# Optimization experiments

Measured on AMD Instinct MI355X. Metric: run time of the kernel, lower is better.

Reference implementation:

```python
import jax, jax.numpy as jnp
import numpy as np

N_CLASSES = 2048
NUM_GROUP = 8
CLS_PER_GROUP = N_CLASSES // NUM_GROUP  # 256
NUM_SAMPLE = 10
EMB_DIM = 400
COMMITMENT = 0.25


def setup_inputs() -> dict:
    key = jax.random.key(0)
    k1, k2 = jax.random.split(key)
    x0 = jax.random.normal(k1, (64, 512, 1, EMB_DIM), dtype=jnp.float32)
    emb = jax.random.normal(k2, (N_CLASSES, EMB_DIM), dtype=jnp.float32)
    return {"x0": x0, "emb": emb}


def reference(x0, emb):
    x = x0  # normalize=False path
    M = x0.shape[0] * x0.shape[1] * x0.shape[2]
    x1 = x.reshape(M, EMB_DIM)

    # pairwise squared distances [M, N_CLASSES]
    d = (jnp.sum(x1 ** 2, axis=1, keepdims=True)
         + jnp.sum(emb ** 2, axis=1)
         - 2.0 * x1 @ emb.T)

    # per-group mean distance -> group argmin
    d_g = d.reshape(M, NUM_GROUP, CLS_PER_GROUP)
    group = jnp.argmin(jnp.mean(d_g, axis=2), axis=1)  # [M]

    # inverse-distance probs restricted to the chosen group
    d_sel = jnp.take_along_axis(d_g, group[:, None, None], axis=1)[:, 0, :]  # [M, CLS_PER_GROUP]
    prob_sel = 1.0 / d_sel
    p, idx_local = jax.lax.top_k(prob_sel, NUM_SAMPLE)  # descending, [M, NUM_SAMPLE]
    index = group[:, None] * CLS_PER_GROUP + idx_local  # global codebook indices

    # L1 normalize kept probabilities (F.normalize p=1)
    prob_dist = p / jnp.maximum(jnp.sum(jnp.abs(p), axis=1, keepdims=True), 1e-12)

    # entropy of top-1 code histogram
    hist = jnp.bincount(index[:, 0], length=N_CLASSES).astype(jnp.float32)
    pr = hist / jnp.float32(M)
    entropy = -jnp.sum(jnp.where(hist > 0, pr * jnp.log(jnp.where(hist > 0, pr, 1.0)), 0.0))

    # weighted gather-sum of code vectors (probs are detached in original)
    gathered = emb[index]  # [M, NUM_SAMPLE, EMB_DIM]
    w = jax.lax.stop_gradient(prob_dist)[:, :, None]
    output = jnp.sum(gathered * w, axis=1).reshape(x.shape)

    out0 = jax.lax.stop_gradient(output - x) + x  # straight-through
    q_latent = jnp.mean((jax.lax.stop_gradient(x) - output) ** 2)
    e_latent = jnp.mean((x - jax.lax.stop_gradient(output)) ** 2)
    loss = q_latent + COMMITMENT * e_latent

    encodings = (1.0 / d)[None]  # [1, M, N_CLASSES]
    return (loss, out0, entropy, encodings)
```

## Files before the change

kernel.cpp:

```cpp
#include <hip/hip_runtime.h>
#include <math.h>

#define M_ROWS 32768
#define N_CLS  2048
#define NGRP   8
#define CPG    256
#define NS     10
#define NCAND  16
#define EDIM   400
#define KPAD   416
#define NKT    13
#define BK     32
#define SGS    448
#define NPART  32

typedef _Float16 f16x8 __attribute__((ext_vector_type(8)));
typedef float f32x4 __attribute__((ext_vector_type(4)));

__device__ __forceinline__ void gld_lds16(const void* g, void* l) {
    __builtin_amdgcn_global_load_lds(
        (const __attribute__((address_space(1))) unsigned int*)g,
        (__attribute__((address_space(3))) unsigned int*)l, 16, 0, 0);
}

__global__ __launch_bounds__(256) void k_split_hi(const float* __restrict__ in,
                                                  unsigned short* __restrict__ hi,
                                                  float* __restrict__ ss, int rows) {
    int row  = blockIdx.x * 4 + (threadIdx.x >> 6);
    int lane = threadIdx.x & 63;
    if (row >= rows) return;
    const float* src = in + (size_t)row * EDIM;
    unsigned short* ph = hi + (size_t)row * KPAD;
    float s = 0.f;
    #pragma unroll
    for (int q = 0; q < 2; ++q) {
        int c4 = lane + q * 64;
        if (c4 < KPAD / 4) {
            int k = c4 * 4;
            float4 v = make_float4(0.f, 0.f, 0.f, 0.f);
            if (k < EDIM) v = *(const float4*)(src + k);
            float va[4] = {v.x, v.y, v.z, v.w};
            unsigned short ha[4];
            #pragma unroll
            for (int t = 0; t < 4; ++t) {
                float f = va[t];
                _Float16 h = (_Float16)f;
                ha[t] = __builtin_bit_cast(unsigned short, h);
                s = fmaf(f, f, s);
            }
            ushort4 H; H.x = ha[0]; H.y = ha[1]; H.z = ha[2]; H.w = ha[3];
            *(ushort4*)(ph + k) = H;
        }
    }
    #pragma unroll
    for (int o = 32; o; o >>= 1) s += __shfl_xor(s, o, 64);
    if (lane == 0) ss[row] = s;
}

__global__ __launch_bounds__(448) void k_groupsum(const float* __restrict__ emb,
                                                  const unsigned short* __restrict__ ehi,
                                                  float* __restrict__ Sg,
                                                  float* __restrict__ SgH) {
    const int g = blockIdx.x;
    const int t = threadIdx.x;
    float se = 0.f, sh = 0.f;
    if (t < EDIM) {
        for (int j = 0; j < CPG; ++j) {
            se += emb[(size_t)(g * CPG + j) * EDIM + t];
            _Float16 h = __builtin_bit_cast(_Float16, ehi[(size_t)(g * CPG + j) * KPAD + t]);
            sh += (float)h;
        }
    }
    Sg[g * SGS + t]  = se;
    SgH[g * SGS + t] = sh;
}

__global__ __launch_bounds__(256, 4) void k_dist1(
    const unsigned short* __restrict__ xhi, const unsigned short* __restrict__ ehi,
    const float* __restrict__ xx, const float* __restrict__ ee,
    float* __restrict__ enc, float* __restrict__ gsum) {
    __shared__ __attribute__((aligned(16))) _Float16 Ah[128][BK];
    __shared__ __attribute__((aligned(16))) _Float16 Bh[128][BK];

    const int wg    = blockIdx.x;
    const int xcd   = wg & 7;
    const int local = wg >> 3;
    const int mx    = xcd * 32 + (local & 31);
    const int ny    = local >> 5;
    const int m0    = mx * 128;
    const int n0    = ny * 128;

    const int tid  = threadIdx.x;
    const int lane = tid & 63, wid = tid >> 6;
    const int wr = (wid >> 1) * 64, wc = (wid & 1) * 64;
    const int lr = lane & 15, ko = lane >> 4;

    f32x4 acc[4][4];
    #pragma unroll
    for (int i = 0; i < 4; ++i)
        #pragma unroll
        for (int j = 0; j < 4; ++j) { f32x4 z = {0.f, 0.f, 0.f, 0.f}; acc[i][j] = z; }

    for (int kt = 0; kt < NKT; ++kt) {
        const int k0 = kt * BK;
        #pragma unroll
        for (int q = 0; q < 2; ++q) {
            int c = q * 256 + tid;
            int row = c >> 2, kc = c & 3;
            size_t goA = (size_t)(m0 + row) * KPAD + k0 + kc * 8;
            size_t goB = (size_t)(n0 + row) * KPAD + k0 + kc * 8;
            int loff = (c >> 6) * 1024;
            gld_lds16(xhi + goA, (char*)&Ah[0][0] + loff);
            gld_lds16(ehi + goB, (char*)&Bh[0][0] + loff);
        }
        __syncthreads();

        f16x8 a_h[4];
        #pragma unroll
        for (int i = 0; i < 4; ++i)
            a_h[i] = *(const f16x8*)&Ah[wr + i * 16 + lr][ko * 8];
        #pragma unroll
        for (int j = 0; j < 4; ++j) {
            f16x8 b_h = *(const f16x8*)&Bh[wc + j * 16 + lr][ko * 8];
            #pragma unroll
            for (int i = 0; i < 4; ++i)
                acc[i][j] = __builtin_amdgcn_mfma_f32_16x16x32_f16(a_h[i], b_h, acc[i][j], 0, 0, 0);
        }
        __syncthreads();
    }

    #pragma unroll
    for (int i = 0; i < 4; ++i) {
        #pragma unroll
        for (int r = 0; r < 4; ++r) {
            int row = m0 + wr + i * 16 + ko * 4 + r;
            float xm = xx[row];
            float rs = 0.f;
            #pragma unroll
            for (int j = 0; j < 4; ++j) {
                int col = n0 + wc + j * 16 + lr;
                float dd = fmaf(-2.f, acc[i][j][r], xm + ee[col]);
                rs += dd;
                enc[(size_t)row * N_CLS + col] = 1.0f / dd;
            }
            rs += __shfl_xor(rs, 1, 64);
            rs += __shfl_xor(rs, 2, 64);
            rs += __shfl_xor(rs, 4, 64);
            rs += __shfl_xor(rs, 8, 64);
            if (lr == 0)
                gsum[(size_t)row * NPART + ny * 2 + (wc >> 6)] = rs;
        }
    }
}

__global__ __launch_bounds__(256) void k_select4(const float* __restrict__ x,
                                                 const float* __restrict__ emb,
                                                 const float* __restrict__ enc,
                                                 const float* __restrict__ gsum,
                                                 const float* __restrict__ Sg,
                                                 const float* __restrict__ SgH,
                                                 const float* __restrict__ xx,
                                                 const float* __restrict__ ee,
                                                 float* __restrict__ out0,
                                                 float* __restrict__ rmse,
                                                 unsigned int* __restrict__ hist) {
    const int wave = threadIdx.x >> 6;
    const int lane = threadIdx.x & 63;
    const int m = blockIdx.x * 4 + wave;

    const float* xrg = x + (size_t)m * EDIM;
    float xr[7], xh[7];
    #pragma unroll
    for (int k = 0; k < 7; ++k) {
        int d = lane + 64 * k;
        float f = (d < EDIM) ? xrg[d] : 0.f;
        xr[k] = f;
        xh[k] = (float)(_Float16)f;
    }
    const float xm = xx[m];

    float aD[NGRP];
    #pragma unroll
    for (int g = 0; g < NGRP; ++g) aD[g] = 0.f;
    #pragma unroll
    for (int k = 0; k < 7; ++k) {
        int d = lane + 64 * k;
        #pragma unroll
        for (int g = 0; g < NGRP; ++g) {
            aD[g] = fmaf(xr[k], Sg[g * SGS + d], aD[g]);
            aD[g] = fmaf(-xh[k], SgH[g * SGS + d], aD[g]);
        }
    }
    #pragma unroll
    for (int g = 0; g < NGRP; ++g) {
        aD[g] += __shfl_xor(aD[g], 8, 64);
        aD[g] += __shfl_xor(aD[g], 16, 64);
        aD[g] += __shfl_xor(aD[g], 32, 64);
    }
    const int myg = (lane >> 3) & 7;
    float s = aD[0];
    s = (myg == 1) ? aD[1] : s;
    s = (myg == 2) ? aD[2] : s;
    s = (myg == 3) ? aD[3] : s;
    s = (myg == 4) ? aD[4] : s;
    s = (myg == 5) ? aD[5] : s;
    s = (myg == 6) ? aD[6] : s;
    s = (myg == 7) ? aD[7] : s;
    s += __shfl_xor(s, 1, 64);
    s += __shfl_xor(s, 2, 64);
    s += __shfl_xor(s, 4, 64);
    const float* gs = gsum + (size_t)m * NPART;
    float base = gs[myg * 4 + 0] + gs[myg * 4 + 1] + gs[myg * 4 + 2] + gs[myg * 4 + 3];
    float sc = fmaf(-2.f, s, base);
    int bg = myg; float bv = sc;
    #pragma unroll
    for (int o = 8; o < 64; o <<= 1) {
        float ov = __shfl_xor(bv, o, 64);
        int   og = __shfl_xor(bg, o, 64);
        if (ov < bv || (ov == bv && og < bg)) { bv = ov; bg = og; }
    }
    const int j0 = bg * CPG;

    const float* pr = enc + (size_t)m * N_CLS + j0;
    float4 pv4 = *(const float4*)(pr + lane * 4);
    unsigned key0 = (__float_as_uint(pv4.x) & 0xFFFFFF00u) | (255u - (unsigned)(lane * 4 + 0));
    unsigned key1 = (__float_as_uint(pv4.y) & 0xFFFFFF00u) | (255u - (unsigned)(lane * 4 + 1));
    unsigned key2 = (__float_as_uint(pv4.z) & 0xFFFFFF00u) | (255u - (unsigned)(lane * 4 + 2));
    unsigned key3 = (__float_as_uint(pv4.w) & 0xFFFFFF00u) | (255u - (unsigned)(lane * 4 + 3));

    unsigned candKey = 0;
    #pragma unroll
    for (int t = 0; t < NCAND; ++t) {
        unsigned a01 = key0 > key1 ? key0 : key1;
        unsigned a23 = key2 > key3 ? key2 : key3;
        unsigned mk  = a01 > a23 ? a01 : a23;
        #pragma unroll
        for (int o = 1; o < 64; o <<= 1) {
            unsigned ok = (unsigned)__shfl_xor((int)mk, o, 64);
            mk = ok > mk ? ok : mk;
        }
        if (lane == t) candKey = mk;
        unsigned widx = 255u - (mk & 0xFFu);
        if ((widx >> 2) == (unsigned)lane) {
            unsigned slot = widx & 3u;
            key0 = (slot == 0u) ? 0u : key0;
            key1 = (slot == 1u) ? 0u : key1;
            key2 = (slot == 2u) ? 0u : key2;
            key3 = (slot == 3u) ? 0u : key3;
        }
    }
    int cand = 255 - (int)(candKey & 0xFFu);

    int cj = __shfl(cand, lane >> 2, 64);
    int jg = j0 + cj;
    const float4* er4 = (const float4*)(emb + (size_t)jg * EDIM);
    const float4* xs4 = (const float4*)xrg;
    float a = 0.f;
    #pragma unroll
    for (int q = 0; q < 25; ++q) {
        int idx = (lane & 3) + 4 * q;
        float4 e = er4[idx];
        float4 xv = xs4[idx];
        a = fmaf(xv.x, e.x, a);
        a = fmaf(xv.y, e.y, a);
        a = fmaf(xv.z, e.z, a);
        a = fmaf(xv.w, e.w, a);
    }
    a += __shfl_xor(a, 1, 64);
    a += __shfl_xor(a, 2, 64);
    float dd = fmaf(-2.f, a, xm + ee[jg]);
    float pvq = 1.0f / dd;
    float pcur = __shfl(pvq, (lane & 15) * 4, 64);
    int   ccur = __shfl(cand, lane & 15, 64);

    const int l16 = lane & 15;
    #pragma unroll
    for (int k = 2; k <= 16; k <<= 1) {
        #pragma unroll
        for (int j = k >> 1; j > 0; j >>= 1) {
            float opv = __shfl_xor(pcur, j, 16);
            int   occ = __shfl_xor(ccur, j, 16);
            bool amLow     = (l16 & j) == 0;
            bool blockDesc = (l16 & k) == 0;
            bool iGreater  = (pcur > opv) || (pcur == opv && ccur < occ);
            bool keep = (amLow == blockDesc) ? iGreater : !iGreater;
            if (!keep) { pcur = opv; ccur = occ; }
        }
    }

    float ps = (l16 < NS) ? pcur : 0.f;
    ps += __shfl_xor(ps, 1, 16);
    ps += __shfl_xor(ps, 2, 16);
    ps += __shfl_xor(ps, 4, 16);
    ps += __shfl_xor(ps, 8, 16);
    float wn = fmaxf(ps, 1e-12f);

    if (lane == 0) atomicAdd(&hist[j0 + ccur], 1u);

    float wt[NS]; int gt[NS];
    #pragma unroll
    for (int t = 0; t < NS; ++t) {
        wt[t] = __shfl(pcur, t, 16) / wn;
        gt[t] = j0 + __shfl(ccur, t, 16);
    }
    float* orow = out0 + (size_t)m * EDIM;
    float sq = 0.f;
    #pragma unroll
    for (int k = 0; k < 7; ++k) {
        int d = lane + 64 * k;
        if (d < EDIM) {
            float o = 0.f;
            #pragma unroll
            for (int t = 0; t < NS; ++t) o = fmaf(wt[t], emb[(size_t)gt[t] * EDIM + d], o);
            float xv = xr[k];
            float diff = xv - o;
            sq = fmaf(diff, diff, sq);
            orow[d] = (o - xv) + xv;
        }
    }
    #pragma unroll
    for (int o = 32; o; o >>= 1) sq += __shfl_xor(sq, o, 64);
    if (lane == 0) rmse[m] = sq;
}

__global__ __launch_bounds__(1024) void k_final(const float* __restrict__ rmse,
                                                const unsigned int* __restrict__ hist,
                                                float* __restrict__ loss_out,
                                                float* __restrict__ ent_out) {
    __shared__ float red[1024];
    const int t = threadIdx.x;

    float s = 0.f;
    for (int i = t; i < M_ROWS; i += 1024) s += rmse[i];
    red[t] = s; __syncthreads();
    for (int off = 512; off; off >>= 1) {
        if (t < off) red[t] += red[t + off];
        __syncthreads();
    }
    if (t == 0) {
        float q = red[0] / 13107200.0f;
        loss_out[0] = q + 0.25f * q;
    }
    __syncthreads();

    float e = 0.f;
    for (int i = t; i < N_CLS; i += 1024) {
        unsigned int h = hist[i];
        if (h > 0) {
            float prb = (float)h / 32768.0f;
            e -= prb * logf(prb);
        }
    }
    red[t] = e; __syncthreads();
    for (int off = 512; off; off >>= 1) {
        if (t < off) red[t] += red[t + off];
        __syncthreads();
    }
    if (t == 0) ent_out[0] = red[0];
}

extern "C" void kernel_launch(void* const* d_in, const int* in_sizes, int n_in,
                              void* d_out, int out_size, void* d_ws, size_t ws_size,
                              hipStream_t stream) {
    const float* x   = (const float*)d_in[0];
    const float* emb = (const float*)d_in[1];

    float* out      = (float*)d_out;
    float* loss_out = out;
    float* out0     = out + 1;
    float* ent_out  = out + 1 + M_ROWS * EDIM;
    float* enc      = out + 2 + M_ROWS * EDIM;

    float* ws   = (float*)d_ws;
    float* ee   = ws;
    float* xx   = ee + N_CLS;
    float* Sg   = xx + M_ROWS;
    float* SgH  = Sg + NGRP * SGS;
    float* gsum = SgH + NGRP * SGS;
    float* rmse = gsum + (size_t)M_ROWS * NPART;
    unsigned int* hist = (unsigned int*)(rmse + M_ROWS);
    float* fend = rmse + M_ROWS + N_CLS;

    unsigned short* xhi = (unsigned short*)fend;
    unsigned short* ehi = xhi + (size_t)M_ROWS * KPAD;

    hipMemsetAsync(hist, 0, N_CLS * sizeof(unsigned int), stream);

    k_split_hi<<<M_ROWS / 4, 256, 0, stream>>>(x, xhi, xx, M_ROWS);
    k_split_hi<<<N_CLS / 4, 256, 0, stream>>>(emb, ehi, ee, N_CLS);
    k_groupsum<<<NGRP, 448, 0, stream>>>(emb, ehi, Sg, SgH);

    k_dist1<<<(M_ROWS / 128) * (N_CLS / 128), 256, 0, stream>>>(xhi, ehi, xx, ee, enc, gsum);

    k_select4<<<M_ROWS / 4, 256, 0, stream>>>(x, emb, enc, gsum, Sg, SgH, xx, ee,
                                              out0, rmse, hist);

    k_final<<<1, 1024, 0, stream>>>(rmse, hist, loss_out, ent_out);
}
```

Baseline: 360.0 us.

## Double-buffer LDS tiles in distance GEMM and use DPP for warp reductions

The distance GEMM kernel now double-buffers its A/B LDS tiles. It issues the next K-tile's global-to-LDS loads before computing the current tile and waits with an explicit vmcnt count and a raw s_barrier, so load latency can overlap the MFMA work. Separately, many xor-shuffle reductions and the bitonic sort steps in the selection kernel switch to DPP row permutes for offsets 1, 2 and 8, avoiding ds_bpermute LDS traffic. The tradeoff is double the LDS footprint and reliance on a hand-set vmcnt value and DPP control encodings being correct.

```diff
diff --git a/kernel.cpp b/kernel.cpp
--- a/kernel.cpp
+++ b/kernel.cpp
@@ -21,6 +21,35 @@
     __builtin_amdgcn_global_load_lds(
         (const __attribute__((address_space(1))) unsigned int*)g,
         (__attribute__((address_space(3))) unsigned int*)l, 16, 0, 0);
+}
+
+#define DPP_X1 0xB1
+#define DPP_X2 0x4E
+#define DPP_X8 0x128
+
+template <int CTRL>
+__device__ __forceinline__ int dpp_i(int v) {
+    return __builtin_amdgcn_update_dpp(v, v, CTRL, 0xF, 0xF, true);
+}
+template <int CTRL>
+__device__ __forceinline__ float dpp_f(float v) {
+    return __builtin_bit_cast(float,
+        __builtin_amdgcn_update_dpp(__builtin_bit_cast(int, v),
+                                    __builtin_bit_cast(int, v), CTRL, 0xF, 0xF, true));
+}
+template <int J>
+__device__ __forceinline__ float xch_f(float v) {
+    if constexpr (J == 1) return dpp_f<DPP_X1>(v);
+    else if constexpr (J == 2) return dpp_f<DPP_X2>(v);
+    else if constexpr (J == 8) return dpp_f<DPP_X8>(v);
+    else return __shfl_xor(v, J, 64);
+}
+template <int J>
+__device__ __forceinline__ int xch_i(int v) {
+    if constexpr (J == 1) return dpp_i<DPP_X1>(v);
+    else if constexpr (J == 2) return dpp_i<DPP_X2>(v);
+    else if constexpr (J == 8) return dpp_i<DPP_X8>(v);
+    else return __shfl_xor(v, J, 64);
 }
 
 __global__ __launch_bounds__(256) void k_split_hi(const float* __restrict__ in,
@@ -79,8 +108,8 @@
     const unsigned short* __restrict__ xhi, const unsigned short* __restrict__ ehi,
     const float* __restrict__ xx, const float* __restrict__ ee,
     float* __restrict__ enc, float* __restrict__ gsum) {
-    __shared__ __attribute__((aligned(16))) _Float16 Ah[128][BK];
-    __shared__ __attribute__((aligned(16))) _Float16 Bh[128][BK];
+    __shared__ __attribute__((aligned(16))) _Float16 Ah[2][128][BK];
+    __shared__ __attribute__((aligned(16))) _Float16 Bh[2][128][BK];
 
     const int wg    = blockIdx.x;
     const int xcd   = wg & 7;
@@ -95,38 +124,48 @@
     const int wr = (wid >> 1) * 64, wc = (wid & 1) * 64;
     const int lr = lane & 15, ko = lane >> 4;
 
+    auto stage = [&](int b, int kt) {
+        const int k0 = kt * BK;
+        #pragma unroll
+        for (int q = 0; q < 2; ++q) {
+            int cc = q * 256 + tid;
+            int rw = cc >> 2, kc = cc & 3;
+            size_t goA = (size_t)(m0 + rw) * KPAD + k0 + kc * 8;
+            size_t goB = (size_t)(n0 + rw) * KPAD + k0 + kc * 8;
+            int loff = (cc >> 6) * 1024;
+            gld_lds16(xhi + goA, (char*)&Ah[b][0][0] + loff);
+            gld_lds16(ehi + goB, (char*)&Bh[b][0][0] + loff);
+        }
+    };
+
     f32x4 acc[4][4];
     #pragma unroll
     for (int i = 0; i < 4; ++i)
         #pragma unroll
         for (int j = 0; j < 4; ++j) { f32x4 z = {0.f, 0.f, 0.f, 0.f}; acc[i][j] = z; }
 
+    stage(0, 0);
     for (int kt = 0; kt < NKT; ++kt) {
-        const int k0 = kt * BK;
-        #pragma unroll
-        for (int q = 0; q < 2; ++q) {
-            int c = q * 256 + tid;
-            int row = c >> 2, kc = c & 3;
-            size_t goA = (size_t)(m0 + row) * KPAD + k0 + kc * 8;
-            size_t goB = (size_t)(n0 + row) * KPAD + k0 + kc * 8;
-            int loff = (c >> 6) * 1024;
-            gld_lds16(xhi + goA, (char*)&Ah[0][0] + loff);
-            gld_lds16(ehi + goB, (char*)&Bh[0][0] + loff);
-        }
-        __syncthreads();
+        const int cur = kt & 1;
+        if (kt + 1 < NKT) {
+            stage(cur ^ 1, kt + 1);
+            asm volatile("s_waitcnt vmcnt(4)\n\ts_barrier" ::: "memory");
+        } else {
+            asm volatile("s_waitcnt vmcnt(0)\n\ts_barrier" ::: "memory");
+        }
 
         f16x8 a_h[4];
         #pragma unroll
         for (int i = 0; i < 4; ++i)
-            a_h[i] = *(const f16x8*)&Ah[wr + i * 16 + lr][ko * 8];
+            a_h[i] = *(const f16x8*)&Ah[cur][wr + i * 16 + lr][ko * 8];
         #pragma unroll
         for (int j = 0; j < 4; ++j) {
-            f16x8 b_h = *(const f16x8*)&Bh[wc + j * 16 + lr][ko * 8];
+            f16x8 b_h = *(const f16x8*)&Bh[cur][wc + j * 16 + lr][ko * 8];
             #pragma unroll
             for (int i = 0; i < 4; ++i)
                 acc[i][j] = __builtin_amdgcn_mfma_f32_16x16x32_f16(a_h[i], b_h, acc[i][j], 0, 0, 0);
         }
-        __syncthreads();
+        asm volatile("s_barrier" ::: "memory");
     }
 
     #pragma unroll
@@ -143,17 +182,17 @@
                 rs += dd;
                 enc[(size_t)row * N_CLS + col] = 1.0f / dd;
             }
-            rs += __shfl_xor(rs, 1, 64);
-            rs += __shfl_xor(rs, 2, 64);
+            rs += dpp_f<DPP_X1>(rs);
+            rs += dpp_f<DPP_X2>(rs);
             rs += __shfl_xor(rs, 4, 64);
-            rs += __shfl_xor(rs, 8, 64);
+            rs += dpp_f<DPP_X8>(rs);
             if (lr == 0)
                 gsum[(size_t)row * NPART + ny * 2 + (wc >> 6)] = rs;
         }
     }
 }
 
-__global__ __launch_bounds__(256) void k_select4(const float* __restrict__ x,
+__global__ __launch_bounds__(256) void k_select5(const float* __restrict__ x,
                                                  const float* __restrict__ emb,
                                                  const float* __restrict__ enc,
                                                  const float* __restrict__ gsum,
@@ -193,7 +232,7 @@
     }
     #pragma unroll
     for (int g = 0; g < NGRP; ++g) {
-        aD[g] += __shfl_xor(aD[g], 8, 64);
+        aD[g] += dpp_f<DPP_X8>(aD[g]);
         aD[g] += __shfl_xor(aD[g], 16, 64);
         aD[g] += __shfl_xor(aD[g], 32, 64);
     }
@@ -206,15 +245,19 @@
     s = (myg == 5) ? aD[5] : s;
     s = (myg == 6) ? aD[6] : s;
     s = (myg == 7) ? aD[7] : s;
-    s += __shfl_xor(s, 1, 64);
-    s += __shfl_xor(s, 2, 64);
+    s += dpp_f<DPP_X1>(s);
+    s += dpp_f<DPP_X2>(s);
     s += __shfl_xor(s, 4, 64);
     const float* gs = gsum + (size_t)m * NPART;
     float base = gs[myg * 4 + 0] + gs[myg * 4 + 1] + gs[myg * 4 + 2] + gs[myg * 4 + 3];
     float sc = fmaf(-2.f, s, base);
     int bg = myg; float bv = sc;
-    #pragma unroll
-    for (int o = 8; o < 64; o <<= 1) {
+    {
+        float ov = dpp_f<DPP_X8>(bv); int og = dpp_i<DPP_X8>(bg);
+        if (ov < bv || (ov == bv && og < bg)) { bv = ov; bg = og; }
+    }
+    #pragma unroll
+    for (int o = 16; o < 64; o <<= 1) {
         float ov = __shfl_xor(bv, o, 64);
         int   og = __shfl_xor(bg, o, 64);
         if (ov < bv || (ov == bv && og < bg)) { bv = ov; bg = og; }
@@ -234,11 +277,12 @@
         unsigned a01 = key0 > key1 ? key0 : key1;
         unsigned a23 = key2 > key3 ? key2 : key3;
         unsigned mk  = a01 > a23 ? a01 : a23;
-        #pragma unroll
-        for (int o = 1; o < 64; o <<= 1) {
-            unsigned ok = (unsigned)__shfl_xor((int)mk, o, 64);
-            mk = ok > mk ? ok : mk;
-        }
+        { unsigned o = (unsigned)dpp_i<DPP_X1>((int)mk); mk = o > mk ? o : mk; }
+        { unsigned o = (unsigned)dpp_i<DPP_X2>((int)mk); mk = o > mk ? o : mk; }
+        { unsigned o = (unsigned)__shfl_xor((int)mk, 4, 64); mk = o > mk ? o : mk; }
+        { unsigned o = (unsigned)dpp_i<DPP_X8>((int)mk); mk = o > mk ? o : mk; }
+        { unsigned o = (unsigned)__shfl_xor((int)mk, 16, 64); mk = o > mk ? o : mk; }
+        { unsigned o = (unsigned)__shfl_xor((int)mk, 32, 64); mk = o > mk ? o : mk; }
         if (lane == t) candKey = mk;
         unsigned widx = 255u - (mk & 0xFFu);
         if ((widx >> 2) == (unsigned)lane) {
@@ -266,33 +310,32 @@
         a = fmaf(xv.z, e.z, a);
         a = fmaf(xv.w, e.w, a);
     }
-    a += __shfl_xor(a, 1, 64);
-    a += __shfl_xor(a, 2, 64);
+    a += dpp_f<DPP_X1>(a);
+    a += dpp_f<DPP_X2>(a);
     float dd = fmaf(-2.f, a, xm + ee[jg]);
     float pvq = 1.0f / dd;
     float pcur = __shfl(pvq, (lane & 15) * 4, 64);
     int   ccur = __shfl(cand, lane & 15, 64);
 
     const int l16 = lane & 15;
-    #pragma unroll
-    for (int k = 2; k <= 16; k <<= 1) {
-        #pragma unroll
-        for (int j = k >> 1; j > 0; j >>= 1) {
-            float opv = __shfl_xor(pcur, j, 16);
-            int   occ = __shfl_xor(ccur, j, 16);
-            bool amLow     = (l16 & j) == 0;
-            bool blockDesc = (l16 & k) == 0;
-            bool iGreater  = (pcur > opv) || (pcur == opv && ccur < occ);
-            bool keep = (amLow == blockDesc) ? iGreater : !iGreater;
-            if (!keep) { pcur = opv; ccur = occ; }
-        }
-    }
+#define BSTEP(K_, J_) { \
+        float opv = xch_f<J_>(pcur); int occ = xch_i<J_>(ccur); \
+        bool amLow     = (l16 & (J_)) == 0; \
+        bool blockDesc = (l16 & (K_)) == 0; \
+        bool iGreater  = (pcur > opv) || (pcur == opv && ccur < occ); \
+        bool keep = (amLow == blockDesc) ? iGreater : !iGreater; \
+        if (!keep) { pcur = opv; ccur = occ; } }
+    BSTEP(2, 1)
+    BSTEP(4, 2) BSTEP(4, 1)
+    BSTEP(8, 4) BSTEP(8, 2) BSTEP(8, 1)
+    BSTEP(16, 8) BSTEP(16, 4) BSTEP(16, 2) BSTEP(16, 1)
+#undef BSTEP
 
     float ps = (l16 < NS) ? pcur : 0.f;
-    ps += __shfl_xor(ps, 1, 16);
-    ps += __shfl_xor(ps, 2, 16);
-    ps += __shfl_xor(ps, 4, 16);
-    ps += __shfl_xor(ps, 8, 16);
+    ps += dpp_f<DPP_X1>(ps);
+    ps += dpp_f<DPP_X2>(ps);
+    ps += __shfl_xor(ps, 4, 64);
+    ps += dpp_f<DPP_X8>(ps);
     float wn = fmaxf(ps, 1e-12f);
 
     if (lane == 0) atomicAdd(&hist[j0 + ccur], 1u);
@@ -318,8 +361,12 @@
             orow[d] = (o - xv) + xv;
         }
     }
-    #pragma unroll
-    for (int o = 32; o; o >>= 1) sq += __shfl_xor(sq, o, 64);
+    sq += dpp_f<DPP_X1>(sq);
+    sq += dpp_f<DPP_X2>(sq);
+    sq += __shfl_xor(sq, 4, 64);
+    sq += dpp_f<DPP_X8>(sq);
+    sq += __shfl_xor(sq, 16, 64);
+    sq += __shfl_xor(sq, 32, 64);
     if (lane == 0) rmse[m] = sq;
 }
 
@@ -392,7 +439,7 @@
 
     k_dist1<<<(M_ROWS / 128) * (N_CLS / 128), 256, 0, stream>>>(xhi, ehi, xx, ee, enc, gsum);
 
-    k_select4<<<M_ROWS / 4, 256, 0, stream>>>(x, emb, enc, gsum, Sg, SgH, xx, ee,
+    k_select5<<<M_ROWS / 4, 256, 0, stream>>>(x, emb, enc, gsum, Sg, SgH, xx, ee,
                                               out0, rmse, hist);
 
     k_final<<<1, 1024, 0, stream>>>(rmse, hist, loss_out, ent_out);
```

Result: faster. 347.9 us (-3.4%).
